# Kernel optimization log

Hardware: AMD Instinct MI355X
Metric: run time of the kernel (lower is better)

Reference implementation:

```python
import jax, jax.numpy as jnp
import numpy as np

N_NODES = 100000
N_EDGES = 1600000  # random edges; self-loops appended -> 1.7M total
NFEATS, NHIDS, NCLASSES = 512, 256, 40


def _spmm(edge_row, edge_col, edge_val, dense):
    # out[r] += val * dense[c]  (COO spmm)
    msgs = edge_val[:, None] * dense[edge_col]           # [E, F]
    return jax.ops.segment_sum(msgs, edge_row, num_segments=N_NODES)


def setup_inputs() -> dict:
    key = jax.random.key(0)
    ks = jax.random.split(key, 8)
    x = jax.random.normal(ks[0], (N_NODES, NFEATS), dtype=jnp.float32)
    stdv1 = 1.0 / np.sqrt(NHIDS)
    W1 = jax.random.uniform(ks[1], (NFEATS, NHIDS), minval=-stdv1, maxval=stdv1, dtype=jnp.float32)
    b1 = jax.random.uniform(ks[2], (NHIDS,), minval=-stdv1, maxval=stdv1, dtype=jnp.float32)
    stdv2 = 1.0 / np.sqrt(NCLASSES)
    W2 = jax.random.uniform(ks[3], (NHIDS, NCLASSES), minval=-stdv2, maxval=stdv2, dtype=jnp.float32)
    b2 = jax.random.uniform(ks[4], (NCLASSES,), minval=-stdv2, maxval=stdv2, dtype=jnp.float32)

    # random adjacency edges + self-loops (normalized_adj does adj = I + adj)
    r = jax.random.randint(ks[5], (N_EDGES,), 0, N_NODES, dtype=jnp.int32)
    c = jax.random.randint(ks[6], (N_EDGES,), 0, N_NODES, dtype=jnp.int32)
    sl = jnp.arange(N_NODES, dtype=jnp.int32)
    edge_row = jnp.concatenate([r, sl])
    edge_col = jnp.concatenate([c, sl])
    raw_val = jnp.ones(edge_row.shape[0], dtype=jnp.float32)
    # deg = row-sum of (A + I); symmetric normalization D^-1/2 (A+I) D^-1/2
    deg = jax.ops.segment_sum(raw_val, edge_row, num_segments=N_NODES)
    dinv = jnp.power(deg, -0.5)
    dinv = jnp.where(jnp.isfinite(dinv), dinv, 0.0)
    edge_val = dinv[edge_row] * raw_val * dinv[edge_col]
    return {"x": x, "W1": W1, "b1": b1, "W2": W2, "b2": b2,
            "edge_row": edge_row, "edge_col": edge_col, "edge_val": edge_val}


def reference(x, W1, b1, W2, b2, edge_row, edge_col, edge_val):
    # layer 1: relu(spmm(adj, x@W1) + b1); dropout skipped (eval mode)
    h = jax.nn.relu(_spmm(edge_row, edge_col, edge_val, x @ W1) + b1)
    # layer 2: spmm(adj, h@W2) + b2
    out = _spmm(edge_row, edge_col, edge_val, h @ W2) + b2
    return out
```

## Files before the change

### kernel.cpp

```cpp
#include <hip/hip_runtime.h>
#include <hip/hip_bf16.h>


#define NFEATS 512
#define NHIDS  256
#define NCLS   40
#define NCLSP  64

typedef unsigned short ushort_t;
typedef unsigned int uint_t;
typedef __attribute__((ext_vector_type(8))) short frag8;
typedef __attribute__((ext_vector_type(4))) float floatx4;

__device__ __forceinline__ ushort_t f2b(float f) {
    uint_t u = __float_as_uint(f);
    uint_t r = (u + 0x7fffu + ((u >> 16) & 1u)) >> 16;
    return (ushort_t)r;
}
__device__ __forceinline__ float b2f(ushort_t b) {
    return __uint_as_float((uint_t)b << 16);
}


__global__ void hist_kernel(const int* __restrict__ row, int* __restrict__ cnt, int E) {
    int e = blockIdx.x * blockDim.x + threadIdx.x;
    if (e < E) atomicAdd(&cnt[row[e]], 1);
}

#define PS_T 256
#define PS_C 4
#define PS_CHUNK (PS_T * PS_C)

__global__ __launch_bounds__(PS_T) void scan_partial_kernel(const int* __restrict__ cnt,
                                                            int* __restrict__ blockSums, int N) {
    __shared__ int sm[PS_T];
    int t = threadIdx.x;
    int base = blockIdx.x * PS_CHUNK + t * PS_C;
    int s = 0;
    if (base + PS_C <= N) {
        int4 v = *(const int4*)(cnt + base);
        s = v.x + v.y + v.z + v.w;
    } else {
        for (int i = 0; i < PS_C; i++) if (base + i < N) s += cnt[base + i];
    }
    sm[t] = s;
    __syncthreads();
    for (int off = PS_T / 2; off > 0; off >>= 1) {
        if (t < off) sm[t] += sm[t + off];
        __syncthreads();
    }
    if (t == 0) blockSums[blockIdx.x] = sm[0];
}

#define SS_T 128
__global__ __launch_bounds__(SS_T) void scan_sums_kernel(int* __restrict__ blockSums, int B) {
    __shared__ int sm[SS_T];
    int t = threadIdx.x;
    int v = (t < B) ? blockSums[t] : 0;
    sm[t] = v;
    __syncthreads();
    for (int off = 1; off < SS_T; off <<= 1) {
        int x = (t >= off) ? sm[t - off] : 0;
        __syncthreads();
        sm[t] += x;
        __syncthreads();
    }
    if (t < B) blockSums[t] = sm[t] - v;
}

__global__ __launch_bounds__(PS_T) void scan_finalize_kernel(int* __restrict__ cnt,
                                                             const int* __restrict__ blockSums,
                                                             int* __restrict__ row_ptr, int N, int E) {
    __shared__ int sm[PS_T];
    int t = threadIdx.x;
    int base = blockIdx.x * PS_CHUNK + t * PS_C;
    int vals[PS_C];
    int s = 0;
#pragma unroll
    for (int i = 0; i < PS_C; i++) {
        int idx = base + i;
        vals[i] = (idx < N) ? cnt[idx] : 0;
        s += vals[i];
    }
    sm[t] = s;
    __syncthreads();
    for (int off = 1; off < PS_T; off <<= 1) {
        int x = (t >= off) ? sm[t - off] : 0;
        __syncthreads();
        sm[t] += x;
        __syncthreads();
    }
    int run = blockSums[blockIdx.x] + sm[t] - s;
#pragma unroll
    for (int i = 0; i < PS_C; i++) {
        int idx = base + i;
        if (idx < N) {
            row_ptr[idx] = run;
            run += vals[i];
            cnt[idx] = 0;
        }
    }
    if (blockIdx.x == 0 && t == 0) row_ptr[N] = E;
}

__global__ void scatter_kernel(const int* __restrict__ row, const int* __restrict__ col,
                               const float* __restrict__ val, const int* __restrict__ row_ptr,
                               int* __restrict__ fill, int2* __restrict__ cv, int E) {
    int e = blockIdx.x * blockDim.x + threadIdx.x;
    if (e < E) {
        int r = row[e];
        int p = row_ptr[r] + atomicAdd(&fill[r], 1);
        cv[p] = make_int2(col[e], __float_as_int(val[e]));
    }
}


__global__ void convert_w1(const float* __restrict__ W1, ushort_t* __restrict__ W1t) {
    int idx = blockIdx.x * 256 + threadIdx.x;
    int k = idx >> 8, n = idx & 255;
    W1t[n * 512 + k] = f2b(W1[idx]);
}

__global__ void convert_w2(const float* __restrict__ W2, ushort_t* __restrict__ W2t) {
    int idx = blockIdx.x * 256 + threadIdx.x;
    int n = idx >> 8, k = idx & 255;
    W2t[idx] = (n < NCLS) ? f2b(W2[k * NCLS + n]) : (ushort_t)0;
}


#define G1_BM 64
#define G1_BN 256
#define G1_BK 32
#define LDK   40

__global__ __launch_bounds__(256) void gemm1_kernel(const float* __restrict__ A,
                                                    const ushort_t* __restrict__ Bt,
                                                    ushort_t* __restrict__ H1, int M) {
    __shared__ ushort_t As[G1_BM * LDK];
    __shared__ ushort_t Bs[G1_BN * LDK];
    int tid  = threadIdx.x;
    int wave = tid >> 6, lane = tid & 63;
    int quad = lane >> 4, ln = lane & 15;
    int m0 = blockIdx.x * G1_BM;

    floatx4 acc[4][4] = {};

    for (int k0 = 0; k0 < NFEATS; k0 += G1_BK) {
#pragma unroll
        for (int i = 0; i < 2; i++) {
            int idx = i * 256 + tid;
            int row = idx >> 3;
            int c4  = idx & 7;
            float4 v = make_float4(0.f, 0.f, 0.f, 0.f);
            int gr = m0 + row;
            if (gr < M) v = *(const float4*)(A + (size_t)gr * NFEATS + k0 + c4 * 4);
            ushort4 b;
            b.x = f2b(v.x); b.y = f2b(v.y); b.z = f2b(v.z); b.w = f2b(v.w);
            *(ushort4*)&As[row * LDK + c4 * 4] = b;
        }
#pragma unroll
        for (int i = 0; i < 4; i++) {
            int idx = i * 256 + tid;
            int n  = idx >> 2;
            int k8 = idx & 3;
            uint4 v = *(const uint4*)(Bt + (size_t)n * 512 + k0 + k8 * 8);
            *(uint4*)&Bs[n * LDK + k8 * 8] = v;
        }
        __syncthreads();
        frag8 af[4], bf[4];
#pragma unroll
        for (int t = 0; t < 4; t++)
            af[t] = *(const frag8*)&As[(t * 16 + ln) * LDK + quad * 8];
#pragma unroll
        for (int t = 0; t < 4; t++)
            bf[t] = *(const frag8*)&Bs[(wave * 64 + t * 16 + ln) * LDK + quad * 8];
#pragma unroll
        for (int mt = 0; mt < 4; mt++)
#pragma unroll
            for (int nt = 0; nt < 4; nt++)
                acc[mt][nt] = __builtin_amdgcn_mfma_f32_16x16x32_bf16(af[mt], bf[nt], acc[mt][nt], 0, 0, 0);
        __syncthreads();
    }
#pragma unroll
    for (int mt = 0; mt < 4; mt++) {
#pragma unroll
        for (int i = 0; i < 4; i++) {
            int m = m0 + mt * 16 + quad * 4 + i;
            if (m < M) {
#pragma unroll
                for (int nt = 0; nt < 4; nt++) {
                    H1[(size_t)m * NHIDS + wave * 64 + nt * 16 + ln] = f2b(acc[mt][nt][i]);
                }
            }
        }
    }
}


__global__ __launch_bounds__(256) void spmm1_kernel(const int* __restrict__ row_ptr,
                                                    const int2* __restrict__ cv,
                                                    const ushort_t* __restrict__ H1,
                                                    const float* __restrict__ b1,
                                                    ushort_t* __restrict__ AGG, int N) {
    int wave = threadIdx.x >> 6, lane = threadIdx.x & 63;
    int r = blockIdx.x * 4 + wave;
    if (r >= N) return;
    int s = row_ptr[r], e = row_ptr[r + 1];
    float a0 = 0.f, a1 = 0.f, a2 = 0.f, a3 = 0.f;
    int j = s;
    for (; j + 3 < e; j += 4) {
        int2 p0 = cv[j];
        int2 p1 = cv[j + 1];
        int2 p2 = cv[j + 2];
        int2 p3 = cv[j + 3];
        ushort4 h0 = *(const ushort4*)(H1 + (size_t)p0.x * NHIDS + lane * 4);
        ushort4 h1 = *(const ushort4*)(H1 + (size_t)p1.x * NHIDS + lane * 4);
        ushort4 h2 = *(const ushort4*)(H1 + (size_t)p2.x * NHIDS + lane * 4);
        ushort4 h3 = *(const ushort4*)(H1 + (size_t)p3.x * NHIDS + lane * 4);
        float v0 = __int_as_float(p0.y), v1 = __int_as_float(p1.y);
        float v2 = __int_as_float(p2.y), v3 = __int_as_float(p3.y);
        a0 += v0 * b2f(h0.x); a1 += v0 * b2f(h0.y); a2 += v0 * b2f(h0.z); a3 += v0 * b2f(h0.w);
        a0 += v1 * b2f(h1.x); a1 += v1 * b2f(h1.y); a2 += v1 * b2f(h1.z); a3 += v1 * b2f(h1.w);
        a0 += v2 * b2f(h2.x); a1 += v2 * b2f(h2.y); a2 += v2 * b2f(h2.z); a3 += v2 * b2f(h2.w);
        a0 += v3 * b2f(h3.x); a1 += v3 * b2f(h3.y); a2 += v3 * b2f(h3.z); a3 += v3 * b2f(h3.w);
    }
    for (; j < e; j++) {
        int2 p0 = cv[j];
        ushort4 h0 = *(const ushort4*)(H1 + (size_t)p0.x * NHIDS + lane * 4);
        float v0 = __int_as_float(p0.y);
        a0 += v0 * b2f(h0.x); a1 += v0 * b2f(h0.y); a2 += v0 * b2f(h0.z); a3 += v0 * b2f(h0.w);
    }
    float4 bb = *(const float4*)(b1 + lane * 4);
    a0 += bb.x; a1 += bb.y; a2 += bb.z; a3 += bb.w;
    ushort4 o;
    o.x = f2b(a0 > 0.f ? a0 : 0.f);
    o.y = f2b(a1 > 0.f ? a1 : 0.f);
    o.z = f2b(a2 > 0.f ? a2 : 0.f);
    o.w = f2b(a3 > 0.f ? a3 : 0.f);
    *(ushort4*)&AGG[(size_t)r * NHIDS + lane * 4] = o;
}


__global__ __launch_bounds__(256) void gemm2_kernel(const ushort_t* __restrict__ AGG,
                                                    const ushort_t* __restrict__ W2t,
                                                    ushort_t* __restrict__ H2, int M) {
    int tid  = threadIdx.x;
    int wave = tid >> 6, lane = tid & 63;
    int quad = lane >> 4, ln = lane & 15;
    int m0 = blockIdx.x * 256 + wave * 64;

    floatx4 acc[4][4] = {};
    frag8 zf = {};

#pragma unroll
    for (int k0 = 0; k0 < NHIDS; k0 += 32) {
        frag8 af[4], bf[4];
#pragma unroll
        for (int mt = 0; mt < 4; mt++) {
            int m = m0 + mt * 16 + ln;
            af[mt] = (m < M) ? *(const frag8*)(AGG + (size_t)m * NHIDS + k0 + quad * 8) : zf;
        }
#pragma unroll
        for (int nt = 0; nt < 4; nt++)
            bf[nt] = *(const frag8*)(W2t + (size_t)(nt * 16 + ln) * NHIDS + k0 + quad * 8);
#pragma unroll
        for (int mt = 0; mt < 4; mt++)
#pragma unroll
            for (int nt = 0; nt < 4; nt++)
                acc[mt][nt] = __builtin_amdgcn_mfma_f32_16x16x32_bf16(af[mt], bf[nt], acc[mt][nt], 0, 0, 0);
    }
#pragma unroll
    for (int mt = 0; mt < 4; mt++) {
#pragma unroll
        for (int i = 0; i < 4; i++) {
            int m = m0 + mt * 16 + quad * 4 + i;
            if (m < M) {
#pragma unroll
                for (int nt = 0; nt < 4; nt++)
                    H2[(size_t)m * NCLSP + nt * 16 + ln] = f2b(acc[mt][nt][i]);
            }
        }
    }
}


__global__ __launch_bounds__(256) void spmm2_kernel(const int* __restrict__ row_ptr,
                                                    const int2* __restrict__ cv,
                                                    const ushort_t* __restrict__ H2,
                                                    const float* __restrict__ b2,
                                                    float* __restrict__ out, int N) {
    int wave = threadIdx.x >> 6, lane = threadIdx.x & 63;
    int half = lane >> 5, fl = lane & 31;
    int r = blockIdx.x * 8 + wave * 2 + half;
    if (r >= N) return;
    int s = row_ptr[r], e = row_ptr[r + 1];
    float a0 = 0.f, a1 = 0.f;
    int j = s;
    for (; j + 1 < e; j += 2) {
        int2 p0 = cv[j];
        int2 p1 = cv[j + 1];
        float v0 = __int_as_float(p0.y);
        float v1 = __int_as_float(p1.y);
        uint_t h0 = *(const uint_t*)(H2 + (size_t)p0.x * NCLSP + fl * 2);
        uint_t h1 = *(const uint_t*)(H2 + (size_t)p1.x * NCLSP + fl * 2);
        a0 += v0 * b2f((ushort_t)(h0 & 0xffff));
        a1 += v0 * b2f((ushort_t)(h0 >> 16));
        a0 += v1 * b2f((ushort_t)(h1 & 0xffff));
        a1 += v1 * b2f((ushort_t)(h1 >> 16));
    }
    if (j < e) {
        int2 p = cv[j];
        float v = __int_as_float(p.y);
        uint_t h = *(const uint_t*)(H2 + (size_t)p.x * NCLSP + fl * 2);
        a0 += v * b2f((ushort_t)(h & 0xffff));
        a1 += v * b2f((ushort_t)(h >> 16));
    }
    if (fl < NCLS / 2) {
        float2 o;
        o.x = a0 + b2[fl * 2];
        o.y = a1 + b2[fl * 2 + 1];
        *(float2*)(out + (size_t)r * NCLS + fl * 2) = o;
    }
}


static inline size_t align256(size_t x) { return (x + 255) & ~(size_t)255; }

extern "C" void kernel_launch(void* const* d_in, const int* in_sizes, int n_in,
                              void* d_out, int out_size, void* d_ws, size_t ws_size,
                              hipStream_t stream) {
    const float* x        = (const float*)d_in[0];
    const float* W1       = (const float*)d_in[1];
    const float* b1       = (const float*)d_in[2];
    const float* W2       = (const float*)d_in[3];
    const float* b2       = (const float*)d_in[4];
    const int*   edge_row = (const int*)d_in[5];
    const int*   edge_col = (const int*)d_in[6];
    const float* edge_val = (const float*)d_in[7];
    float* out = (float*)d_out;

    int N = in_sizes[0] / NFEATS;
    int E = in_sizes[5];

    char* w = (char*)d_ws;
    size_t off = 0;
    ushort_t* H1   = (ushort_t*)(w + off); off += align256((size_t)N * NHIDS * 2);
    ushort_t* AGG  = (ushort_t*)(w + off); off += align256((size_t)N * NHIDS * 2);
    ushort_t* H2   = (ushort_t*)(w + off); off += align256((size_t)N * NCLSP * 2);
    ushort_t* W1t  = (ushort_t*)(w + off); off += align256((size_t)NHIDS * NFEATS * 2);
    ushort_t* W2t  = (ushort_t*)(w + off); off += align256((size_t)NCLSP * NHIDS * 2);
    int*      row_ptr = (int*)(w + off); off += align256((size_t)(N + 1) * 4);
    int*      cnt     = (int*)(w + off); off += align256((size_t)N * 4);
    int*      blockSums = (int*)(w + off); off += align256((size_t)SS_T * 4);
    int2*     cv      = (int2*)(w + off); off += align256((size_t)E * 8);

    int scanB = (N + PS_CHUNK - 1) / PS_CHUNK;

    hipMemsetAsync(cnt, 0, (size_t)N * 4, stream);
    hist_kernel<<<(E + 255) / 256, 256, 0, stream>>>(edge_row, cnt, E);
    convert_w1<<<(NFEATS * NHIDS) / 256, 256, 0, stream>>>(W1, W1t);
    convert_w2<<<(NCLSP * NHIDS) / 256, 256, 0, stream>>>(W2, W2t);
    scan_partial_kernel<<<scanB, PS_T, 0, stream>>>(cnt, blockSums, N);
    scan_sums_kernel<<<1, SS_T, 0, stream>>>(blockSums, scanB);
    scan_finalize_kernel<<<scanB, PS_T, 0, stream>>>(cnt, blockSums, row_ptr, N, E);
    scatter_kernel<<<(E + 255) / 256, 256, 0, stream>>>(edge_row, edge_col, edge_val,
                                                        row_ptr, cnt, cv, E);

    gemm1_kernel<<<(N + G1_BM - 1) / G1_BM, 256, 0, stream>>>(x, W1t, H1, N);
    spmm1_kernel<<<(N + 3) / 4, 256, 0, stream>>>(row_ptr, cv, H1, b1, AGG, N);

    gemm2_kernel<<<(N + 255) / 256, 256, 0, stream>>>(AGG, W2t, H2, N);
    spmm2_kernel<<<(N + 7) / 8, 256, 0, stream>>>(row_ptr, cv, H2, b2, out, N);
}
```

Before: 705.2 us.

## Double-buffer A tile in gemm1 and load B fragments directly from global

The gemm1 kernel now double-buffers the converted A tile in shared memory, prefetching the next K-slice into registers while MFMAs run on the current one, which leaves one barrier per iteration. The B (W1t) tile is no longer staged through shared memory; each wave loads its MFMA fragments straight from global or L2. This targets the load-then-sync stalls of the single-buffered loop, in exchange for more global traffic for B and a heavier register load.

Measured after the change: 697.7 us. Within noise of the previous version (-1.1%).

```diff
diff --git a/kernel.cpp b/kernel.cpp
--- a/kernel.cpp
+++ b/kernel.cpp
@@ -131,56 +131,71 @@
 #define G1_BM 64
 #define G1_BN 256
 #define G1_BK 32
+#define G1_NK (NFEATS / G1_BK)
 #define LDK   40
 
 __global__ __launch_bounds__(256) void gemm1_kernel(const float* __restrict__ A,
                                                     const ushort_t* __restrict__ Bt,
                                                     ushort_t* __restrict__ H1, int M) {
-    __shared__ ushort_t As[G1_BM * LDK];
-    __shared__ ushort_t Bs[G1_BN * LDK];
+    __shared__ ushort_t As[2][G1_BM * LDK];
     int tid  = threadIdx.x;
     int wave = tid >> 6, lane = tid & 63;
     int quad = lane >> 4, ln = lane & 15;
     int m0 = blockIdx.x * G1_BM;
 
+    int srow = tid >> 3;
+    int sc4  = tid & 7;
+    const float* ap0 = A + (size_t)(m0 + srow)      * NFEATS + sc4 * 4;
+    const float* ap1 = A + (size_t)(m0 + srow + 32) * NFEATS + sc4 * 4;
+    bool ok0 = (m0 + srow)      < M;
+    bool ok1 = (m0 + srow + 32) < M;
+    float4 z4 = make_float4(0.f, 0.f, 0.f, 0.f);
+
+    const ushort_t* bbase = Bt + ((size_t)(wave * 64 + ln) * NFEATS) + quad * 8;
+
     floatx4 acc[4][4] = {};
 
-    for (int k0 = 0; k0 < NFEATS; k0 += G1_BK) {
-#pragma unroll
-        for (int i = 0; i < 2; i++) {
-            int idx = i * 256 + tid;
-            int row = idx >> 3;
-            int c4  = idx & 7;
-            float4 v = make_float4(0.f, 0.f, 0.f, 0.f);
-            int gr = m0 + row;
-            if (gr < M) v = *(const float4*)(A + (size_t)gr * NFEATS + k0 + c4 * 4);
-            ushort4 b;
-            b.x = f2b(v.x); b.y = f2b(v.y); b.z = f2b(v.z); b.w = f2b(v.w);
-            *(ushort4*)&As[row * LDK + c4 * 4] = b;
-        }
-#pragma unroll
-        for (int i = 0; i < 4; i++) {
-            int idx = i * 256 + tid;
-            int n  = idx >> 2;
-            int k8 = idx & 3;
-            uint4 v = *(const uint4*)(Bt + (size_t)n * 512 + k0 + k8 * 8);
-            *(uint4*)&Bs[n * LDK + k8 * 8] = v;
-        }
-        __syncthreads();
-        frag8 af[4], bf[4];
-#pragma unroll
-        for (int t = 0; t < 4; t++)
-            af[t] = *(const frag8*)&As[(t * 16 + ln) * LDK + quad * 8];
-#pragma unroll
-        for (int t = 0; t < 4; t++)
-            bf[t] = *(const frag8*)&Bs[(wave * 64 + t * 16 + ln) * LDK + quad * 8];
+    {
+        float4 v0 = ok0 ? *(const float4*)ap0 : z4;
+        float4 v1 = ok1 ? *(const float4*)ap1 : z4;
+        ushort4 b0, b1;
+        b0.x = f2b(v0.x); b0.y = f2b(v0.y); b0.z = f2b(v0.z); b0.w = f2b(v0.w);
+        b1.x = f2b(v1.x); b1.y = f2b(v1.y); b1.z = f2b(v1.z); b1.w = f2b(v1.w);
+        *(ushort4*)&As[0][srow * LDK + sc4 * 4]        = b0;
+        *(ushort4*)&As[0][(srow + 32) * LDK + sc4 * 4] = b1;
+    }
+    __syncthreads();
+
+#pragma unroll 2
+    for (int t = 0; t < G1_NK; ++t) {
+        int cur = t & 1;
+        float4 n0 = z4, n1 = z4;
+        if (t < G1_NK - 1) {
+            if (ok0) n0 = *(const float4*)(ap0 + (t + 1) * G1_BK);
+            if (ok1) n1 = *(const float4*)(ap1 + (t + 1) * G1_BK);
+        }
+        frag8 bfr[4], af[4];
+#pragma unroll
+        for (int nt = 0; nt < 4; nt++)
+            bfr[nt] = *(const frag8*)(bbase + (size_t)nt * 16 * NFEATS + t * G1_BK);
 #pragma unroll
         for (int mt = 0; mt < 4; mt++)
+            af[mt] = *(const frag8*)&As[cur][(mt * 16 + ln) * LDK + quad * 8];
+#pragma unroll
+        for (int mt = 0; mt < 4; mt++)
 #pragma unroll
             for (int nt = 0; nt < 4; nt++)
-                acc[mt][nt] = __builtin_amdgcn_mfma_f32_16x16x32_bf16(af[mt], bf[nt], acc[mt][nt], 0, 0, 0);
-        __syncthreads();
-    }
+                acc[mt][nt] = __builtin_amdgcn_mfma_f32_16x16x32_bf16(af[mt], bfr[nt], acc[mt][nt], 0, 0, 0);
+        if (t < G1_NK - 1) {
+            ushort4 b0, b1;
+            b0.x = f2b(n0.x); b0.y = f2b(n0.y); b0.z = f2b(n0.z); b0.w = f2b(n0.w);
+            b1.x = f2b(n1.x); b1.y = f2b(n1.y); b1.z = f2b(n1.z); b1.w = f2b(n1.w);
+            *(ushort4*)&As[cur ^ 1][srow * LDK + sc4 * 4]        = b0;
+            *(ushort4*)&As[cur ^ 1][(srow + 32) * LDK + sc4 * 4] = b1;
+        }
+        __syncthreads();
+    }
+
 #pragma unroll
     for (int mt = 0; mt < 4; mt++) {
 #pragma unroll
```

## Load GEMM1 fragments directly from global memory and unroll SpMM2 gather by four

Applied to the files above, without the earlier changes.

The first GEMM no longer stages A and B tiles through shared memory with barriers. Each lane now loads its MFMA fragments straight from global memory, converts A to bf16 in registers, and clamps out-of-range rows to avoid bounds checks. This is meant to remove LDS traffic and synchronisation, but it adds redundant global loads, since B is re-read by every block and A is read with poor coalescing. Separately, the second SpMM's edge loop is unrolled from two to four edges to keep more gathers in flight.

After: 752.6 us. +6.7%, slower.

```diff
diff --git a/kernel.cpp b/kernel.cpp
--- a/kernel.cpp
+++ b/kernel.cpp
@@ -129,15 +129,10 @@
 
 
 #define G1_BM 64
-#define G1_BN 256
-#define G1_BK 32
-#define LDK   40
 
 __global__ __launch_bounds__(256) void gemm1_kernel(const float* __restrict__ A,
                                                     const ushort_t* __restrict__ Bt,
                                                     ushort_t* __restrict__ H1, int M) {
-    __shared__ ushort_t As[G1_BM * LDK];
-    __shared__ ushort_t Bs[G1_BN * LDK];
     int tid  = threadIdx.x;
     int wave = tid >> 6, lane = tid & 63;
     int quad = lane >> 4, ln = lane & 15;
@@ -145,42 +140,40 @@
 
     floatx4 acc[4][4] = {};
 
-    for (int k0 = 0; k0 < NFEATS; k0 += G1_BK) {
-#pragma unroll
-        for (int i = 0; i < 2; i++) {
-            int idx = i * 256 + tid;
-            int row = idx >> 3;
-            int c4  = idx & 7;
-            float4 v = make_float4(0.f, 0.f, 0.f, 0.f);
-            int gr = m0 + row;
-            if (gr < M) v = *(const float4*)(A + (size_t)gr * NFEATS + k0 + c4 * 4);
-            ushort4 b;
-            b.x = f2b(v.x); b.y = f2b(v.y); b.z = f2b(v.z); b.w = f2b(v.w);
-            *(ushort4*)&As[row * LDK + c4 * 4] = b;
-        }
-#pragma unroll
-        for (int i = 0; i < 4; i++) {
-            int idx = i * 256 + tid;
-            int n  = idx >> 2;
-            int k8 = idx & 3;
-            uint4 v = *(const uint4*)(Bt + (size_t)n * 512 + k0 + k8 * 8);
-            *(uint4*)&Bs[n * LDK + k8 * 8] = v;
-        }
-        __syncthreads();
-        frag8 af[4], bf[4];
-#pragma unroll
-        for (int t = 0; t < 4; t++)
-            af[t] = *(const frag8*)&As[(t * 16 + ln) * LDK + quad * 8];
-#pragma unroll
-        for (int t = 0; t < 4; t++)
-            bf[t] = *(const frag8*)&Bs[(wave * 64 + t * 16 + ln) * LDK + quad * 8];
+    const ushort_t* bbase = Bt + (size_t)(wave * 64 + ln) * NFEATS + quad * 8;
+
+    const float* abase[4];
+#pragma unroll
+    for (int mt = 0; mt < 4; mt++) {
+        int m = m0 + mt * 16 + ln;
+        if (m > M - 1) m = M - 1;
+        abase[mt] = A + (size_t)m * NFEATS + quad * 8;
+    }
+
+#pragma unroll
+    for (int t = 0; t < NFEATS / 32; ++t) {
+        frag8 af[4], bfr[4];
+#pragma unroll
+        for (int nt = 0; nt < 4; nt++)
+            bfr[nt] = *(const frag8*)(bbase + (size_t)nt * 16 * NFEATS + t * 32);
+#pragma unroll
+        for (int mt = 0; mt < 4; mt++) {
+            float4 lo = *(const float4*)(abase[mt] + t * 32);
+            float4 hi = *(const float4*)(abase[mt] + t * 32 + 4);
+            frag8 f;
+            f[0] = (short)f2b(lo.x); f[1] = (short)f2b(lo.y);
+            f[2] = (short)f2b(lo.z); f[3] = (short)f2b(lo.w);
+            f[4] = (short)f2b(hi.x); f[5] = (short)f2b(hi.y);
+            f[6] = (short)f2b(hi.z); f[7] = (short)f2b(hi.w);
+            af[mt] = f;
+        }
 #pragma unroll
         for (int mt = 0; mt < 4; mt++)
 #pragma unroll
             for (int nt = 0; nt < 4; nt++)
-                acc[mt][nt] = __builtin_amdgcn_mfma_f32_16x16x32_bf16(af[mt], bf[nt], acc[mt][nt], 0, 0, 0);
-        __syncthreads();
-    }
+                acc[mt][nt] = __builtin_amdgcn_mfma_f32_16x16x32_bf16(af[mt], bfr[nt], acc[mt][nt], 0, 0, 0);
+    }
+
 #pragma unroll
     for (int mt = 0; mt < 4; mt++) {
 #pragma unroll
@@ -296,19 +289,29 @@
     int s = row_ptr[r], e = row_ptr[r + 1];
     float a0 = 0.f, a1 = 0.f;
     int j = s;
-    for (; j + 1 < e; j += 2) {
+    for (; j + 3 < e; j += 4) {
         int2 p0 = cv[j];
         int2 p1 = cv[j + 1];
+        int2 p2 = cv[j + 2];
+        int2 p3 = cv[j + 3];
         float v0 = __int_as_float(p0.y);
         float v1 = __int_as_float(p1.y);
+        float v2 = __int_as_float(p2.y);
+        float v3 = __int_as_float(p3.y);
         uint_t h0 = *(const uint_t*)(H2 + (size_t)p0.x * NCLSP + fl * 2);
         uint_t h1 = *(const uint_t*)(H2 + (size_t)p1.x * NCLSP + fl * 2);
+        uint_t h2 = *(const uint_t*)(H2 + (size_t)p2.x * NCLSP + fl * 2);
+        uint_t h3 = *(const uint_t*)(H2 + (size_t)p3.x * NCLSP + fl * 2);
         a0 += v0 * b2f((ushort_t)(h0 & 0xffff));
         a1 += v0 * b2f((ushort_t)(h0 >> 16));
         a0 += v1 * b2f((ushort_t)(h1 & 0xffff));
         a1 += v1 * b2f((ushort_t)(h1 >> 16));
-    }
-    if (j < e) {
+        a0 += v2 * b2f((ushort_t)(h2 & 0xffff));
+        a1 += v2 * b2f((ushort_t)(h2 >> 16));
+        a0 += v3 * b2f((ushort_t)(h3 & 0xffff));
+        a1 += v3 * b2f((ushort_t)(h3 >> 16));
+    }
+    for (; j < e; j++) {
         int2 p = cv[j];
         float v = __int_as_float(p.y);
         uint_t h = *(const uint_t*)(H2 + (size_t)p.x * NCLSP + fl * 2);
```
